# Kernel tuning notes

Hardware: AMD Instinct MI355X
Metric: run time of the kernel (lower is better)

## Reference

```python
import jax, jax.numpy as jnp
import numpy as np

N_NODES = 20000
N_EDGES = 320000
F_IN = 256      # feature_size
H1, C1 = 8, 128 # conv1: heads=8, out=128, concat -> 1024
H2, C2 = 1, 128 # conv2: heads=1, out=emb_size, concat=False
NEG_SLOPE = 0.2


def setup_inputs() -> dict:
    key = jax.random.key(0)
    ks = jax.random.split(key, 10)
    x = jax.random.normal(ks[0], (N_NODES, F_IN), dtype=jnp.float32)
    edge_index = jax.random.randint(ks[1], (2, N_EDGES), 0, N_NODES, dtype=jnp.int64)
    s1 = 1.0 / np.sqrt(F_IN)
    s2 = 1.0 / np.sqrt(H1 * C1)
    W1 = jax.random.uniform(ks[2], (F_IN, H1 * C1), jnp.float32, -s1, s1)
    att_src1 = jax.random.uniform(ks[3], (H1, C1), jnp.float32, -s1, s1)
    att_dst1 = jax.random.uniform(ks[4], (H1, C1), jnp.float32, -s1, s1)
    bias1 = jnp.zeros((H1 * C1,), jnp.float32)
    W2 = jax.random.uniform(ks[5], (H1 * C1, H2 * C2), jnp.float32, -s2, s2)
    att_src2 = jax.random.uniform(ks[6], (H2, C2), jnp.float32, -s2, s2)
    att_dst2 = jax.random.uniform(ks[7], (H2, C2), jnp.float32, -s2, s2)
    bias2 = jnp.zeros((C2,), jnp.float32)
    return {"x": x, "edge_index": edge_index,
            "W1": W1, "att_src1": att_src1, "att_dst1": att_dst1, "bias1": bias1,
            "W2": W2, "att_src2": att_src2, "att_dst2": att_dst2, "bias2": bias2}


def _gat_conv(x, W, a_src, a_dst, bias, src, dst, num_nodes, concat):
    """PyG-style GATConv (eval mode, self-loops already appended to src/dst)."""
    H, C = a_src.shape
    h = (x @ W).reshape(num_nodes, H, C)                     # [N,H,C]
    alpha_src = jnp.sum(h * a_src[None], axis=-1)            # [N,H]
    alpha_dst = jnp.sum(h * a_dst[None], axis=-1)            # [N,H]
    e = alpha_src[src] + alpha_dst[dst]                      # [E,H]
    e = jnp.where(e > 0, e, NEG_SLOPE * e)                   # LeakyReLU(0.2)
    # segment softmax over incoming edges of each dst node
    m = jax.ops.segment_max(e, dst, num_segments=num_nodes)  # [N,H]
    ex = jnp.exp(e - m[dst])
    denom = jax.ops.segment_sum(ex, dst, num_segments=num_nodes)
    alpha = ex / (denom[dst] + 1e-16)                        # [E,H]
    msg = alpha[:, :, None] * h[src]                         # [E,H,C]
    out = jax.ops.segment_sum(msg, dst, num_segments=num_nodes)  # [N,H,C]
    if concat:
        out = out.reshape(num_nodes, H * C)
    else:
        out = out.mean(axis=1)
    return out + bias


def reference(x, edge_index, W1, att_src1, att_dst1, bias1, W2, att_src2, att_dst2, bias2):
    n = x.shape[0]
    loop = jnp.arange(n, dtype=edge_index.dtype)
    src = jnp.concatenate([edge_index[0], loop])
    dst = jnp.concatenate([edge_index[1], loop])
    # dropout layers are identity in eval mode
    h = _gat_conv(x, W1, att_src1, att_dst1, bias1, src, dst, n, concat=True)
    h = jax.nn.elu(h)
    h = _gat_conv(h, W2, att_src2, att_dst2, bias2, src, dst, n, concat=False)
    return jax.nn.log_softmax(h, axis=-1)
```

## Files before the change

### kernel.cpp

```cpp
#include <hip/hip_runtime.h>

#define NN 20000
#define FIN 256
#define D1 1024
#define NH 8
#define C2 128
#define CAP 64

typedef unsigned short u16;
typedef unsigned char u8;
typedef __attribute__((ext_vector_type(8))) short bf16x8;
typedef __attribute__((ext_vector_type(4))) float f32x4;
typedef __attribute__((ext_vector_type(2))) float f32x2;

__device__ __forceinline__ float bf2f(u16 u) {
    return __uint_as_float(((unsigned int)u) << 16);
}
__device__ __forceinline__ u16 f2bf(float f) {
    unsigned int u = __float_as_uint(f);
    u += 0x7FFFu + ((u >> 16) & 1u);
    return (u16)(u >> 16);
}
__device__ __forceinline__ u8 f2fp8(float v) {
    int q = __builtin_amdgcn_cvt_pk_fp8_f32(v, v, 0, false);
    return (u8)(q & 0xFF);
}

__device__ __forceinline__ float bred_max(float v) {
    #pragma unroll
    for (int o = 32; o > 0; o >>= 1) v = fmaxf(v, __shfl_xor(v, o, 64));
    return v;
}
__device__ __forceinline__ float bred_sum(float v) {
    #pragma unroll
    for (int o = 32; o > 0; o >>= 1) v += __shfl_xor(v, o, 64);
    return v;
}

typedef const __attribute__((address_space(1))) unsigned int* as1_u32p;
typedef __attribute__((address_space(3))) unsigned int* as3_u32p;
__device__ __forceinline__ void gload_lds16(const void* g, void* l) {
    __builtin_amdgcn_global_load_lds((as1_u32p)g, (as3_u32p)l, 16, 0, 0);
}

__global__ __launch_bounds__(256) void prep_kernel(const float* __restrict__ x,
                                                   u16* __restrict__ xb,
                                                   const float* __restrict__ W1,
                                                   u16* __restrict__ w1t,
                                                   const float* __restrict__ W2,
                                                   u16* __restrict__ w2t,
                                                   int* __restrict__ cnt) {
    __shared__ float tile[32][33];
    const int b = blockIdx.x, tid = threadIdx.x;
    if (b < 5000) {
        int i = (b * 256 + tid) * 4;
        if (i < NN * FIN) {
            float4 v = *(const float4*)(x + i);
            ushort4 o;
            o.x = f2bf(v.x); o.y = f2bf(v.y); o.z = f2bf(v.z); o.w = f2bf(v.w);
            *(ushort4*)(xb + i) = o;
        }
        return;
    }
    if (b < 5384) {
        const float* in; u16* out; int R, C, bx, by;
        if (b < 5256) {
            int q = b - 5000;
            in = W1; out = w1t; R = FIN; C = D1;
            bx = (q & 31) * 32; by = (q >> 5) * 32;
        } else {
            int q = b - 5256;
            in = W2; out = w2t; R = D1; C = C2;
            bx = (q & 3) * 32; by = (q >> 2) * 32;
        }
        int tx = tid & 31, ty = tid >> 5;
        #pragma unroll
        for (int i = 0; i < 32; i += 8)
            tile[ty + i][tx] = in[(size_t)(by + ty + i) * C + bx + tx];
        __syncthreads();
        #pragma unroll
        for (int i = 0; i < 32; i += 8)
            out[(size_t)(bx + ty + i) * R + by + tx] = f2bf(tile[tx][ty + i]);
        return;
    }
    int i = (b - 5384) * 256 + tid;
    if (i < NN) cnt[i] = 0;
}

template <int BM, int OMODE>
__global__ __launch_bounds__(256) void gemm_mfma(const u16* __restrict__ A,
                                                 const u16* __restrict__ Bt,
                                                 void* __restrict__ C,
                                                 const float* __restrict__ attS,
                                                 const float* __restrict__ attD,
                                                 float* __restrict__ as_out,
                                                 float* __restrict__ ad_out,
                                                 int NHo,
                                                 int M, int N, int K) {
    constexpr int TM = BM / 32;
    __shared__ u16 ldsA[BM * 32];
    __shared__ u16 ldsB[128 * 32];
    __shared__ float asb[BM], adb[BM];
    const int tid = threadIdx.x;
    const int lane = tid & 63, w = tid >> 6;
    const int wr = w >> 1, wc = w & 1;
    const int row0 = blockIdx.x * BM, col0 = blockIdx.y * 128;
    const int head = blockIdx.y;
    const int l15 = lane & 15, quad = lane >> 4;

    for (int t = tid; t < BM; t += 256) { asb[t] = 0.f; adb[t] = 0.f; }

    f32x4 acc[TM][4];
    #pragma unroll
    for (int i = 0; i < TM; i++)
        #pragma unroll
        for (int j = 0; j < 4; j++)
            acc[i][j] = (f32x4){0.f, 0.f, 0.f, 0.f};

    for (int k0 = 0; k0 < K; k0 += 32) {
        #pragma unroll
        for (int i = 0; i < BM / 64; i++) {
            int c = tid + i * 256;
            int r = c >> 2, ko = (c & 3) * 8;
            int gr = row0 + r; if (gr >= M) gr = M - 1;
            gload_lds16(A + (size_t)gr * K + k0 + ko, ldsA + c * 8);
        }
        #pragma unroll
        for (int i = 0; i < 2; i++) {
            int c = tid + i * 256;
            int n = c >> 2, ko = (c & 3) * 8;
            gload_lds16(Bt + (size_t)(col0 + n) * K + k0 + ko, ldsB + c * 8);
        }
        __syncthreads();
        bf16x8 af[TM], bfr[4];
        #pragma unroll
        for (int i = 0; i < TM; i++) {
            int m = wr * (BM / 2) + i * 16 + l15;
            af[i] = *(const bf16x8*)(ldsA + m * 32 + quad * 8);
        }
        #pragma unroll
        for (int j = 0; j < 4; j++) {
            int n = wc * 64 + j * 16 + l15;
            bfr[j] = *(const bf16x8*)(ldsB + n * 32 + quad * 8);
        }
        #pragma unroll
        for (int i = 0; i < TM; i++)
            #pragma unroll
            for (int j = 0; j < 4; j++)
                acc[i][j] = __builtin_amdgcn_mfma_f32_16x16x32_bf16(af[i], bfr[j], acc[i][j], 0, 0, 0);
        __syncthreads();
    }
    #pragma unroll
    for (int i = 0; i < TM; i++) {
        #pragma unroll
        for (int j = 0; j < 4; j++) {
            #pragma unroll
            for (int r = 0; r < 4; r++) {
                int row = row0 + wr * (BM / 2) + i * 16 + quad * 4 + r;
                int col = col0 + wc * 64 + j * 16 + l15;
                if (row < M) {
                    float v = acc[i][j][r];
                    if (OMODE == 1)
                        ((u16*)C)[(size_t)row * N + col] = f2bf(v);
                    else
                        ((u8*)C)[(size_t)row * N + col] = f2fp8(v);
                }
            }
        }
    }
    float attS_r[4], attD_r[4];
    #pragma unroll
    for (int j = 0; j < 4; j++) {
        int col = wc * 64 + j * 16 + l15;
        attS_r[j] = attS[head * 128 + col];
        attD_r[j] = attD[head * 128 + col];
    }
    #pragma unroll
    for (int i = 0; i < TM; i++) {
        #pragma unroll
        for (int r = 0; r < 4; r++) {
            float ps = 0.f, pd = 0.f;
            #pragma unroll
            for (int j = 0; j < 4; j++) {
                float v = acc[i][j][r];
                ps = fmaf(v, attS_r[j], ps);
                pd = fmaf(v, attD_r[j], pd);
            }
            #pragma unroll
            for (int o = 1; o < 16; o <<= 1) {
                ps += __shfl_xor(ps, o, 64);
                pd += __shfl_xor(pd, o, 64);
            }
            if (l15 == 0) {
                int row = wr * (BM / 2) + i * 16 + quad * 4 + r;
                atomicAdd(&asb[row], ps);
                atomicAdd(&adb[row], pd);
            }
        }
    }
    __syncthreads();
    for (int t = tid; t < BM; t += 256) {
        int row = row0 + t;
        if (row < M) {
            as_out[(size_t)row * NHo + head] = asb[t];
            ad_out[(size_t)row * NHo + head] = adb[t];
        }
    }
}

__global__ void fill_kernel(const int* __restrict__ ei, int E, int N,
                            int* __restrict__ cnt,
                            int* __restrict__ csr,
                            const float* __restrict__ as1,
                            const float* __restrict__ ad1,
                            float* __restrict__ pw1) {
    int j = blockIdx.x * 256 + threadIdx.x;
    if (j >= E + N) return;
    int s, d;
    if (j < E) { s = ei[j]; d = ei[E + j]; }
    else { s = j - E; d = j - E; }
    int pos = atomicAdd(&cnt[d], 1);
    if (pos >= CAP) return;
    int slot = d * CAP + pos;
    csr[slot] = s;
    float4 s0 = *(const float4*)(as1 + s * NH);
    float4 s1 = *(const float4*)(as1 + s * NH + 4);
    float4 d0 = *(const float4*)(ad1 + d * NH);
    float4 d1 = *(const float4*)(ad1 + d * NH + 4);
    float e[8] = {s0.x + d0.x, s0.y + d0.y, s0.z + d0.z, s0.w + d0.w,
                  s1.x + d1.x, s1.y + d1.y, s1.z + d1.z, s1.w + d1.w};
    float p[8];
    #pragma unroll
    for (int h = 0; h < 8; h++) {
        float v = e[h] > 0.f ? e[h] : 0.2f * e[h];
        p[h] = __expf(v);
    }
    *(float4*)(pw1 + (size_t)slot * 8) = *(const float4*)p;
    *(float4*)(pw1 + (size_t)slot * 8 + 4) = *(const float4*)(p + 4);
}

#define A1_FETCH8(E0, Q, P)                                                   \
    {                                                                         \
        _Pragma("unroll")                                                     \
        for (int u = 0; u < 8; u++) {                                         \
            int e = (E0) + u;                       \
            int s = __builtin_amdgcn_readlane(idx, e);                        \
            s = s < 0 ? 0 : (s > NN - 1 ? NN - 1 : s);        \
            Q[u] = *(const uint4*)(h1q + (size_t)s * D1 + c0);                \
            P[u] = pwc[e * 8];                       \
        }                                                                     \
        __builtin_amdgcn_sched_barrier(0);                                    \
    }
#define A1_PROC8(E0, Q, P)                                                    \
    {                                                                         \
        _Pragma("unroll")                                                     \
        for (int u = 0; u < 8; u++) {                                         \
            float pp = ((E0) + u < deg) ? (P)[u] : 0.f;                       \
            den += pp;                                                        \
            f32x2 pv2 = {pp, pp};                                             \
            acc[0] += pv2 * __builtin_amdgcn_cvt_pk_f32_fp8((Q)[u].x, false); \
            acc[1] += pv2 * __builtin_amdgcn_cvt_pk_f32_fp8((Q)[u].x, true);  \
            acc[2] += pv2 * __builtin_amdgcn_cvt_pk_f32_fp8((Q)[u].y, false); \
            acc[3] += pv2 * __builtin_amdgcn_cvt_pk_f32_fp8((Q)[u].y, true);  \
            acc[4] += pv2 * __builtin_amdgcn_cvt_pk_f32_fp8((Q)[u].z, false); \
            acc[5] += pv2 * __builtin_amdgcn_cvt_pk_f32_fp8((Q)[u].z, true);  \
            acc[6] += pv2 * __builtin_amdgcn_cvt_pk_f32_fp8((Q)[u].w, false); \
            acc[7] += pv2 * __builtin_amdgcn_cvt_pk_f32_fp8((Q)[u].w, true);  \
        }                                                                     \
    }

__global__ __launch_bounds__(256) void agg1_kernel(const u8* __restrict__ h1q,
                                                   const float* __restrict__ pw1,
                                                   const int* __restrict__ cnt,
                                                   const int* __restrict__ csr,
                                                   const float* __restrict__ bias1,
                                                   u16* __restrict__ x2) {
    const int tid = threadIdx.x;
    const int lane = tid & 63;
    const int dst = (blockIdx.x << 2) + (tid >> 6);
    const int c0 = lane * 16;
    const int h = lane >> 3;
    const int base = dst * CAP;

    int idx = csr[base + lane];
    const int deg = __builtin_amdgcn_readfirstlane(max(1, min(cnt[dst], CAP)));
    const float* pwc = pw1 + (size_t)base * 8 + h;

    f32x2 acc[8];
    #pragma unroll
    for (int k = 0; k < 8; k++) acc[k] = (f32x2){0.f, 0.f};
    float den = 0.f;

    const int nit = (deg + 7) >> 3;
    uint4 qa[8], qb[8];
    float pa[8], pb[8];
    A1_FETCH8(0, qa, pa)
    int g = 0;
    for (; g + 2 < nit; g += 2) {
        A1_FETCH8((g + 1) * 8, qb, pb)
        A1_PROC8(g * 8, qa, pa)
        A1_FETCH8((g + 2) * 8, qa, pa)
        A1_PROC8((g + 1) * 8, qb, pb)
    }
    if (g + 1 < nit) {
        A1_FETCH8((g + 1) * 8, qb, pb)
        A1_PROC8(g * 8, qa, pa)
        A1_PROC8((g + 1) * 8, qb, pb)
    } else {
        A1_PROC8(g * 8, qa, pa)
    }

    float inv = 1.f / (den + 1e-16f);
    u16 ov[16];
    #pragma unroll
    for (int k = 0; k < 8; k++) {
        float a0 = acc[k][0] * inv + bias1[c0 + 2 * k];
        float a1 = acc[k][1] * inv + bias1[c0 + 2 * k + 1];
        a0 = a0 > 0.f ? a0 : (__expf(a0) - 1.f);
        a1 = a1 > 0.f ? a1 : (__expf(a1) - 1.f);
        ov[2 * k] = f2bf(a0);
        ov[2 * k + 1] = f2bf(a1);
    }
    *(uint4*)(x2 + (size_t)dst * D1 + c0) = *(const uint4*)ov;
    *(uint4*)(x2 + (size_t)dst * D1 + c0 + 8) = *(const uint4*)(ov + 8);
}

#define A2_FETCH8(E0, Q)                                                      \
    {                                                                         \
        _Pragma("unroll")                                                     \
        for (int u = 0; u < 8; u++) {                                         \
            int s = __builtin_amdgcn_readlane(idx, (E0) + u);                 \
            s = s < 0 ? 0 : (s > NN - 1 ? NN - 1 : s);                        \
            Q[u] = *(const unsigned int*)(h2 + (size_t)s * C2 + lane2);       \
        }                                                                     \
        __builtin_amdgcn_sched_barrier(0);                                    \
    }
#define A2_PROC8(E0, Q)                                                       \
    {                                                                         \
        _Pragma("unroll")                                                     \
        for (int u = 0; u < 8; u++) {                                         \
            int e = (E0) + u;                                                 \
            float pp = (e < deg) ? __uint_as_float(__builtin_amdgcn_readlane( \
                                       __float_as_uint(pl), e))               \
                                 : 0.f;                                       \
            den += pp;                                                        \
            f32x2 pv2 = {pp, pp};                                             \
            f32x2 f = {__uint_as_float((Q)[u] << 16),                         \
                       __uint_as_float((Q)[u] & 0xFFFF0000u)};                \
            acc += pv2 * f;                                                   \
        }                                                                     \
    }

__global__ __launch_bounds__(256) void agg2_kernel(const u16* __restrict__ h2,
                                                   const float* __restrict__ as2,
                                                   const float* __restrict__ ad2,
                                                   const int* __restrict__ cnt,
                                                   const int* __restrict__ csr,
                                                   const float* __restrict__ bias2,
                                                   float* __restrict__ out) {
    const int tid = threadIdx.x;
    const int lane = tid & 63;
    const int dst = (blockIdx.x << 2) + (tid >> 6);
    const int base = dst * CAP;
    const int lane2 = lane * 2;

    int idx = csr[base + lane];
    const int deg = __builtin_amdgcn_readfirstlane(max(1, min(cnt[dst], CAP)));
    const float adv = ad2[dst];
    int idxc = idx < 0 ? 0 : (idx > NN - 1 ? NN - 1 : idx);
    float ev = as2[idxc] + adv;
    ev = ev > 0.f ? ev : 0.2f * ev;
    float pl = __expf(ev);

    f32x2 acc = {0.f, 0.f};
    float den = 0.f;

    const int nit = (deg + 7) >> 3;
    unsigned int qa[8], qb[8];
    A2_FETCH8(0, qa)
    int g = 0;
    for (; g + 2 < nit; g += 2) {
        A2_FETCH8((g + 1) * 8, qb)
        A2_PROC8(g * 8, qa)
        A2_FETCH8((g + 2) * 8, qa)
        A2_PROC8((g + 1) * 8, qb)
    }
    if (g + 1 < nit) {
        A2_FETCH8((g + 1) * 8, qb)
        A2_PROC8(g * 8, qa)
        A2_PROC8((g + 1) * 8, qb)
    } else {
        A2_PROC8(g * 8, qa)
    }

    float inv = 1.f / (den + 1e-16f);
    float l0 = acc[0] * inv + bias2[lane2];
    float l1 = acc[1] * inv + bias2[lane2 + 1];
    float m = bred_max(fmaxf(l0, l1));
    float ex = bred_sum(__expf(l0 - m) + __expf(l1 - m));
    float lse = m + __logf(ex);
    float2 ov = {l0 - lse, l1 - lse};
    *(float2*)(out + (size_t)dst * C2 + lane2) = ov;
}

extern "C" void kernel_launch(void* const* d_in, const int* in_sizes, int n_in,
                              void* d_out, int out_size, void* d_ws, size_t ws_size,
                              hipStream_t stream) {
    const float* x        = (const float*)d_in[0];
    const int*   ei       = (const int*)d_in[1];
    const float* W1       = (const float*)d_in[2];
    const float* att_src1 = (const float*)d_in[3];
    const float* att_dst1 = (const float*)d_in[4];
    const float* bias1    = (const float*)d_in[5];
    const float* W2       = (const float*)d_in[6];
    const float* att_src2 = (const float*)d_in[7];
    const float* att_dst2 = (const float*)d_in[8];
    const float* bias2    = (const float*)d_in[9];
    float* out = (float*)d_out;
    const int E = in_sizes[1] / 2;

    char* ws = (char*)d_ws;
    size_t off = 0;
    auto alloc = [&](size_t b) {
        void* p = ws + off;
        off += (b + 255) & ~(size_t)255;
        return p;
    };
    u8*  h1q  = (u8*)alloc((size_t)NN * D1);
    u16* x2   = (u16*)alloc((size_t)NN * D1 * 2);
    u16* h2   = (u16*)alloc((size_t)NN * C2 * 2);
    u16* xb   = (u16*)alloc((size_t)NN * FIN * 2);
    u16* w1t  = (u16*)alloc((size_t)D1 * FIN * 2);
    u16* w2t  = (u16*)alloc((size_t)C2 * D1 * 2);
    float* as1 = (float*)alloc((size_t)NN * NH * 4);
    float* ad1 = (float*)alloc((size_t)NN * NH * 4);
    float* as2 = (float*)alloc((size_t)NN * 4);
    float* ad2 = (float*)alloc((size_t)NN * 4);
    int* cnt  = (int*)alloc((size_t)NN * 4);
    int* csr  = (int*)alloc((size_t)NN * CAP * 4);
    float* pw1 = (float*)alloc((size_t)NN * CAP * 8 * 4);

    const int PREP_BLOCKS = 5000 + 256 + 128 + (NN + 255) / 256;
    prep_kernel<<<PREP_BLOCKS, 256, 0, stream>>>(x, xb, W1, w1t, W2, w2t, cnt);

    gemm_mfma<128, 2><<<dim3((NN + 127) / 128, D1 / 128), 256, 0, stream>>>(
        xb, w1t, h1q, att_src1, att_dst1, as1, ad1, NH, NN, D1, FIN);
    fill_kernel<<<(E + NN + 255) / 256, 256, 0, stream>>>(ei, E, NN, cnt, csr,
                                                          as1, ad1, pw1);
    agg1_kernel<<<(NN + 3) / 4, 256, 0, stream>>>(h1q, pw1, cnt, csr, bias1, x2);
    gemm_mfma<64, 1><<<dim3((NN + 63) / 64, C2 / 128), 256, 0, stream>>>(
        x2, w2t, h2, att_src2, att_dst2, as2, ad2, 1, NN, C2, D1);
    agg2_kernel<<<(NN + 3) / 4, 256, 0, stream>>>(h2, as2, ad2, cnt, csr, bias2, out);
}
```

Baseline: 236.8 us.

## Double-buffer GEMM LDS tiles and compute edge attention weights inside aggregation

The GEMM kernel now uses two LDS buffers and issues the global-to-LDS loads for the next K tile before computing on the current one, so load latency overlaps the MFMA work. Separately, fill_kernel no longer precomputes and stores per-edge exp(leakyrelu) weights in a large pw1 buffer. agg1 instead gathers as1[src] and computes the leaky-relu and exp inline, which removes a large write and read of edge weights. The trade-off is recomputed exp work in agg1, an extra scattered gather per edge, and doubled LDS use in the GEMM, which may lower occupancy. The second GEMM loop drops the sync between load and compute and relies on the end-of-iteration barrier, so whether the async LDS loads are complete before they are read is a possible correctness risk.

```diff
diff --git a/kernel.cpp b/kernel.cpp
--- a/kernel.cpp
+++ b/kernel.cpp
@@ -87,6 +87,25 @@
     if (i < NN) cnt[i] = 0;
 }
 
+#define G_STAGE(BUF, K0)                                                   \
+    {                                                                      \
+        _Pragma("unroll")                                                  \
+        for (int i = 0; i < BM / 64; i++) {                                \
+            int c = tid + i * 256;                                         \
+            int r = c >> 2, ko = (c & 3) * 8;                              \
+            int gr = row0 + r; if (gr >= M) gr = M - 1;                    \
+            gload_lds16(A + (size_t)gr * K + (K0) + ko,                    \
+                        &ldsA[BUF][c * 8]);                                \
+        }                                                                  \
+        _Pragma("unroll")                                                  \
+        for (int i = 0; i < 2; i++) {                                      \
+            int c = tid + i * 256;                                         \
+            int n = c >> 2, ko = (c & 3) * 8;                              \
+            gload_lds16(Bt + (size_t)(col0 + n) * K + (K0) + ko,           \
+                        &ldsB[BUF][c * 8]);                                \
+        }                                                                  \
+    }
+
 template <int BM, int OMODE>
 __global__ __launch_bounds__(256) void gemm_mfma(const u16* __restrict__ A,
                                                  const u16* __restrict__ Bt,
@@ -98,8 +117,8 @@
                                                  int NHo,
                                                  int M, int N, int K) {
     constexpr int TM = BM / 32;
-    __shared__ u16 ldsA[BM * 32];
-    __shared__ u16 ldsB[128 * 32];
+    __shared__ u16 ldsA[2][BM * 32];
+    __shared__ u16 ldsB[2][128 * 32];
     __shared__ float asb[BM], adb[BM];
     const int tid = threadIdx.x;
     const int lane = tid & 63, w = tid >> 6;
@@ -117,31 +136,24 @@
         for (int j = 0; j < 4; j++)
             acc[i][j] = (f32x4){0.f, 0.f, 0.f, 0.f};
 
+    G_STAGE(0, 0)
+    __syncthreads();
+    int cur = 0;
     for (int k0 = 0; k0 < K; k0 += 32) {
-        #pragma unroll
-        for (int i = 0; i < BM / 64; i++) {
-            int c = tid + i * 256;
-            int r = c >> 2, ko = (c & 3) * 8;
-            int gr = row0 + r; if (gr >= M) gr = M - 1;
-            gload_lds16(A + (size_t)gr * K + k0 + ko, ldsA + c * 8);
-        }
-        #pragma unroll
-        for (int i = 0; i < 2; i++) {
-            int c = tid + i * 256;
-            int n = c >> 2, ko = (c & 3) * 8;
-            gload_lds16(Bt + (size_t)(col0 + n) * K + k0 + ko, ldsB + c * 8);
-        }
-        __syncthreads();
+        if (k0 + 32 < K) {
+            G_STAGE(cur ^ 1, k0 + 32)
+            __builtin_amdgcn_sched_barrier(0);
+        }
         bf16x8 af[TM], bfr[4];
         #pragma unroll
         for (int i = 0; i < TM; i++) {
             int m = wr * (BM / 2) + i * 16 + l15;
-            af[i] = *(const bf16x8*)(ldsA + m * 32 + quad * 8);
+            af[i] = *(const bf16x8*)(&ldsA[cur][m * 32 + quad * 8]);
         }
         #pragma unroll
         for (int j = 0; j < 4; j++) {
             int n = wc * 64 + j * 16 + l15;
-            bfr[j] = *(const bf16x8*)(ldsB + n * 32 + quad * 8);
+            bfr[j] = *(const bf16x8*)(&ldsB[cur][n * 32 + quad * 8]);
         }
         #pragma unroll
         for (int i = 0; i < TM; i++)
@@ -149,6 +161,7 @@
             for (int j = 0; j < 4; j++)
                 acc[i][j] = __builtin_amdgcn_mfma_f32_16x16x32_bf16(af[i], bfr[j], acc[i][j], 0, 0, 0);
         __syncthreads();
+        cur ^= 1;
     }
     #pragma unroll
     for (int i = 0; i < TM; i++) {
@@ -210,10 +223,7 @@
 
 __global__ void fill_kernel(const int* __restrict__ ei, int E, int N,
                             int* __restrict__ cnt,
-                            int* __restrict__ csr,
-                            const float* __restrict__ as1,
-                            const float* __restrict__ ad1,
-                            float* __restrict__ pw1) {
+                            int* __restrict__ csr) {
     int j = blockIdx.x * 256 + threadIdx.x;
     if (j >= E + N) return;
     int s, d;
@@ -221,22 +231,7 @@
     else { s = j - E; d = j - E; }
     int pos = atomicAdd(&cnt[d], 1);
     if (pos >= CAP) return;
-    int slot = d * CAP + pos;
-    csr[slot] = s;
-    float4 s0 = *(const float4*)(as1 + s * NH);
-    float4 s1 = *(const float4*)(as1 + s * NH + 4);
-    float4 d0 = *(const float4*)(ad1 + d * NH);
-    float4 d1 = *(const float4*)(ad1 + d * NH + 4);
-    float e[8] = {s0.x + d0.x, s0.y + d0.y, s0.z + d0.z, s0.w + d0.w,
-                  s1.x + d1.x, s1.y + d1.y, s1.z + d1.z, s1.w + d1.w};
-    float p[8];
-    #pragma unroll
-    for (int h = 0; h < 8; h++) {
-        float v = e[h] > 0.f ? e[h] : 0.2f * e[h];
-        p[h] = __expf(v);
-    }
-    *(float4*)(pw1 + (size_t)slot * 8) = *(const float4*)p;
-    *(float4*)(pw1 + (size_t)slot * 8 + 4) = *(const float4*)(p + 4);
+    csr[d * CAP + pos] = s;
 }
 
 #define A1_FETCH8(E0, Q, P)                                                   \
@@ -247,7 +242,7 @@
             int s = __builtin_amdgcn_readlane(idx, e);                        \
             s = s < 0 ? 0 : (s > NN - 1 ? NN - 1 : s);        \
             Q[u] = *(const uint4*)(h1q + (size_t)s * D1 + c0);                \
-            P[u] = pwc[e * 8];                       \
+            P[u] = as1[s * NH + h];            \
         }                                                                     \
         __builtin_amdgcn_sched_barrier(0);                                    \
     }
@@ -255,7 +250,9 @@
     {                                                                         \
         _Pragma("unroll")                                                     \
         for (int u = 0; u < 8; u++) {                                         \
-            float pp = ((E0) + u < deg) ? (P)[u] : 0.f;                       \
+            float ev = (P)[u] + adv;                                          \
+            ev = ev > 0.f ? ev : 0.2f * ev;               \
+            float pp = ((E0) + u < deg) ? __expf(ev) : 0.f;                   \
             den += pp;                                                        \
             f32x2 pv2 = {pp, pp};                                             \
             acc[0] += pv2 * __builtin_amdgcn_cvt_pk_f32_fp8((Q)[u].x, false); \
@@ -270,7 +267,8 @@
     }
 
 __global__ __launch_bounds__(256) void agg1_kernel(const u8* __restrict__ h1q,
-                                                   const float* __restrict__ pw1,
+                                                   const float* __restrict__ as1,
+                                                   const float* __restrict__ ad1,
                                                    const int* __restrict__ cnt,
                                                    const int* __restrict__ csr,
                                                    const float* __restrict__ bias1,
@@ -284,7 +282,7 @@
 
     int idx = csr[base + lane];
     const int deg = __builtin_amdgcn_readfirstlane(max(1, min(cnt[dst], CAP)));
-    const float* pwc = pw1 + (size_t)base * 8 + h;
+    const float adv = ad1[dst * NH + h];
 
     f32x2 acc[8];
     #pragma unroll
@@ -438,16 +436,14 @@
     float* ad2 = (float*)alloc((size_t)NN * 4);
     int* cnt  = (int*)alloc((size_t)NN * 4);
     int* csr  = (int*)alloc((size_t)NN * CAP * 4);
-    float* pw1 = (float*)alloc((size_t)NN * CAP * 8 * 4);
 
     const int PREP_BLOCKS = 5000 + 256 + 128 + (NN + 255) / 256;
     prep_kernel<<<PREP_BLOCKS, 256, 0, stream>>>(x, xb, W1, w1t, W2, w2t, cnt);
 
     gemm_mfma<128, 2><<<dim3((NN + 127) / 128, D1 / 128), 256, 0, stream>>>(
         xb, w1t, h1q, att_src1, att_dst1, as1, ad1, NH, NN, D1, FIN);
-    fill_kernel<<<(E + NN + 255) / 256, 256, 0, stream>>>(ei, E, NN, cnt, csr,
-                                                          as1, ad1, pw1);
-    agg1_kernel<<<(NN + 3) / 4, 256, 0, stream>>>(h1q, pw1, cnt, csr, bias1, x2);
+    fill_kernel<<<(E + NN + 255) / 256, 256, 0, stream>>>(ei, E, NN, cnt, csr);
+    agg1_kernel<<<(NN + 3) / 4, 256, 0, stream>>>(h1q, as1, ad1, cnt, csr, bias1, x2);
     gemm_mfma<64, 1><<<dim3((NN + 63) / 64, C2 / 128), 256, 0, stream>>>(
         x2, w2t, h2, att_src2, att_dst2, as2, ad2, 1, NN, C2, D1);
     agg2_kernel<<<(NN + 3) / 4, 256, 0, stream>>>(h2, as2, ad2, cnt, csr, bias2, out);
```

New measurement: 231.2 us. 2.4% less time.
